# Performance work log

Hardware: AMD Instinct MI355X
Metric: run time of the kernel (lower is better)

## Reference

```python
import jax, jax.numpy as jnp
import numpy as np

BQ, BP, L, CIN, H1, H2, COUT = 32, 256, 16, 8192, 256, 32, 8192


def _conv_block(x, w1, b1, w2, b2, w3, b3):
    # x: (B, L, H1) -> Conv1d stack over token dim with residual, as in self.convs
    h = jnp.transpose(x, (0, 2, 1))  # (B, H1, L)
    for w, b in ((w1, b1), (w2, b2), (w3, b3)):
        h = jax.lax.conv_general_dilated(h, w, (1,), [(2, 2)],
                                         dimension_numbers=('NCH', 'OIH', 'NCH'))
        h = jax.nn.relu(h + b[None, :, None])
    return jnp.transpose(h, (0, 2, 1)) + x


def setup_inputs() -> dict:
    key = jax.random.key(0)
    ks = jax.random.split(key, 16)
    query_x = (jax.random.uniform(ks[0], (BQ, L, CIN)) < 0.01).astype(jnp.float32)
    poi_x = (jax.random.uniform(ks[1], (BP, L, CIN)) < 0.01).astype(jnp.float32)
    query_loc = jax.random.uniform(ks[2], (BQ, 2)) * 100.0
    poi_loc = jax.random.uniform(ks[3], (BP, 2)) * 100.0
    enc_w = jax.random.normal(ks[4], (H1, CIN)) * 0.02
    conv_w1 = jax.random.normal(ks[5], (H1, H1, 5)) * 0.02
    conv_w2 = jax.random.normal(ks[6], (H1, H1, 5)) * 0.02
    conv_w3 = jax.random.normal(ks[7], (H1, H1, 5)) * 0.02
    conv_b1 = jnp.zeros((H1,), jnp.float32)
    conv_b2 = jnp.zeros((H1,), jnp.float32)
    conv_b3 = jnp.zeros((H1,), jnp.float32)
    dec_w1 = jax.random.normal(ks[8], (H2, 2 * H1)) * 0.05
    dec_b1 = jnp.zeros((H2,), jnp.float32)
    dec_w2 = jax.random.normal(ks[9], (H2, H2)) * 0.1
    dec_b2 = jnp.zeros((H2,), jnp.float32)
    # torch init fills this with 0; use small randn so the path is non-trivial
    dec_w3 = jax.random.normal(ks[10], (COUT, H2)) * 0.01
    a = jnp.asarray(1.0, jnp.float32)
    b = jnp.asarray(0.0, jnp.float32)
    c = jnp.asarray(1.0, jnp.float32)
    d = jnp.asarray(0.0, jnp.float32)
    return dict(query_x=query_x, query_loc=query_loc, poi_x=poi_x, poi_loc=poi_loc,
                enc_w=enc_w, conv_w1=conv_w1, conv_b1=conv_b1, conv_w2=conv_w2,
                conv_b2=conv_b2, conv_w3=conv_w3, conv_b3=conv_b3,
                dec_w1=dec_w1, dec_b1=dec_b1, dec_w2=dec_w2, dec_b2=dec_b2,
                dec_w3=dec_w3, a=a, b=b, c=c, d=d)


def reference(query_x, query_loc, poi_x, poi_loc, enc_w, conv_w1, conv_b1,
              conv_w2, conv_b2, conv_w3, conv_b3, dec_w1, dec_b1, dec_w2,
              dec_b2, dec_w3, a, b, c, d):
    # --- encode ---
    q_h = _conv_block(query_x @ enc_w.T, conv_w1, conv_b1, conv_w2, conv_b2, conv_w3, conv_b3)
    p_h = _conv_block(poi_x @ enc_w.T, conv_w1, conv_b1, conv_w2, conv_b2, conv_w3, conv_b3)
    q_emb = q_h.mean(axis=1)  # (Bq, H1)
    p_emb = p_h.mean(axis=1)  # (Bp, H1)
    # --- bloom masks ---
    q_bloom = jnp.minimum(query_x.sum(axis=1), 1.0)  # (Bq, 8192)
    p_bloom = jnp.minimum(poi_x.sum(axis=1), 1.0)    # (Bp, 8192)
    interaction = q_bloom[:, None, :] * p_bloom[None, :, :]  # (Bq, Bp, 8192)
    q_bits = q_bloom.sum(axis=-1, keepdims=True)             # (Bq, 1)
    # --- pairwise MLP decode ---
    bq, bp = q_emb.shape[0], p_emb.shape[0]
    all_embed = jnp.concatenate([
        jnp.broadcast_to(q_emb[:, None, :], (bq, bp, q_emb.shape[-1])),
        jnp.broadcast_to(p_emb[None, :, :], (bq, bp, p_emb.shape[-1])),
    ], axis=-1)  # (Bq, Bp, 2*H1)
    h = jax.nn.relu(all_embed)
    h = jax.nn.relu(h @ dec_w1.T + dec_b1)
    h = jax.nn.relu(h @ dec_w2.T + dec_b2)
    w = h @ dec_w3.T  # (Bq, Bp, 8192)
    weights = jnp.where(w >= 0, w, w * 0.125) + 1.0  # LeakyReLU(1/8) + 1
    desc_sim = (interaction * weights).sum(axis=-1) / q_bits  # (Bq, Bp)
    # --- geo-distance fusion ---
    dist = jnp.sqrt(((query_loc[:, None, :] - poi_loc[None, :, :]) ** 2).sum(axis=-1))
    mean = desc_sim.mean(axis=-1, keepdims=True)
    std = jnp.std(desc_sim, axis=-1, keepdims=True, ddof=1)  # torch.std is unbiased
    desc_sim = (desc_sim - mean) / (std + 1e-6)
    dist_sim = -jnp.log(dist + 1.0)
    return (c - jax.nn.sigmoid(a * desc_sim + b)) * (dist_sim - d)
```

## Files before the change

kernel.cpp:

```cpp
#include <hip/hip_runtime.h>

#define NB 288
#define NBQ 32
#define NBP 256
#define LTOK 16
#define CIN 8192
#define H1 256
#define H2 32
#define MASKW 256
#define XROW 264

typedef __attribute__((ext_vector_type(8))) short short8;
typedef __attribute__((ext_vector_type(4))) float f32x4;

__device__ __forceinline__ unsigned short f2bf(float f) {
    unsigned u = __float_as_uint(f);
    u += 0x7fffu + ((u >> 16) & 1u);
    return (unsigned short)(u >> 16);
}

__device__ __forceinline__ float block_reduce_sum_256(float v, float* red) {
    int tid = threadIdx.x;
    red[tid] = v; __syncthreads();
    for (int st = 128; st > 0; st >>= 1) {
        if (tid < st) red[tid] += red[tid + st];
        __syncthreads();
    }
    float r = red[0];
    __syncthreads();
    return r;
}

__global__ __launch_bounds__(256) void k_transpose(const float* __restrict__ w,
                                                   float* __restrict__ wt) {
    __shared__ float tile[32][33];
    int k0 = blockIdx.x * 32;
    int h0 = blockIdx.y * 32;
    int tx = threadIdx.x & 31, ty = threadIdx.x >> 5;
#pragma unroll
    for (int i = 0; i < 32; i += 8)
        tile[ty + i][tx] = w[(h0 + ty + i) * CIN + k0 + tx];
    __syncthreads();
#pragma unroll
    for (int i = 0; i < 32; i += 8)
        wt[(size_t)(k0 + ty + i) * H1 + h0 + tx] = tile[tx][ty + i];
}

__global__ __launch_bounds__(256) void k_wprep(const float* __restrict__ w1,
                                               const float* __restrict__ w2,
                                               const float* __restrict__ w3,
                                               unsigned short* __restrict__ wtb) {
    int bx = blockIdx.x;
    int l = bx / 1280;
    int r = bx - l * 1280;
    int o = r / 5;
    int d = r - o * 5;
    int i = threadIdx.x;
    const float* w = (l == 0) ? w1 : (l == 1) ? w2 : w3;
    wtb[(size_t)l * 327680 + (size_t)o * 1280 + d * 256 + i] =
        f2bf(w[(size_t)o * 1280 + i * 5 + d]);
}

__global__ __launch_bounds__(256) void k_encode(const float* __restrict__ qx,
                                                const float* __restrict__ px,
                                                const float* __restrict__ wt,
                                                float* __restrict__ encoded,
                                                unsigned short* __restrict__ xbuf,
                                                unsigned* __restrict__ masks) {
    int row = blockIdx.x;
    int b = row >> 4;
    const float* x = (b < NBQ) ? (qx + (size_t)row * CIN)
                               : (px + (size_t)(row - NBQ * LTOK) * CIN);
    __shared__ int idxs[2048];
    __shared__ int cnt;
    int tid = threadIdx.x;
    if (tid == 0) cnt = 0;
    __syncthreads();
    const float4* x4 = (const float4*)x;
#pragma unroll
    for (int j = 0; j < 8; ++j) {
        float4 v = x4[j * 256 + tid];
        int base = (j * 256 + tid) * 4;
        float vv[4] = {v.x, v.y, v.z, v.w};
#pragma unroll
        for (int c = 0; c < 4; ++c) {
            if (vv[c] != 0.f) {
                int k = base + c;
                int p = atomicAdd(&cnt, 1);
                if (p < 2048) idxs[p] = k;
                atomicOr(&masks[b * MASKW + (k >> 5)], 1u << (k & 31));
            }
        }
    }
    __syncthreads();
    int n = min(cnt, 2048);
    float acc = 0.f;
#pragma unroll 4
    for (int j = 0; j < n; ++j)
        acc += wt[(size_t)idxs[j] * H1 + tid];
    encoded[(size_t)row * H1 + tid] = acc;
    xbuf[(size_t)row * H1 + tid] = f2bf(acc);
}

__global__ __launch_bounds__(256) void k_qbits(const unsigned* __restrict__ masks,
                                               float* __restrict__ qbits) {
    __shared__ int red[256];
    int q = blockIdx.x, tid = threadIdx.x;
    red[tid] = __popc(masks[q * MASKW + tid]);
    __syncthreads();
    for (int st = 128; st > 0; st >>= 1) {
        if (tid < st) red[tid] += red[tid + st];
        __syncthreads();
    }
    if (tid == 0) qbits[q] = (float)red[0];
}

__global__ __launch_bounds__(256) void k_cgemm(const unsigned short* __restrict__ actIn,
                                               unsigned short* __restrict__ actOut,
                                               float* __restrict__ actOutF,
                                               const unsigned short* __restrict__ wl,
                                               const float* __restrict__ bias,
                                               int last) {
    __shared__ unsigned short Als[4 * 20 * XROW];
    __shared__ unsigned short Bls[64 * XROW];
    int tid = threadIdx.x;
    int m0 = blockIdx.x * 64, n0 = blockIdx.y * 64;

    int* Ai = (int*)Als;
#pragma unroll
    for (int i = tid; i < 4 * 20 * XROW / 2; i += 256) Ai[i] = 0;
    __syncthreads();

    int row = tid >> 2, part = tid & 3;
    {
        const short8* src = (const short8*)(actIn + (size_t)(m0 + row) * 256 + part * 64);
        unsigned short* dst = Als + ((row >> 4) * 20 + (row & 15) + 2) * XROW + part * 64;
#pragma unroll
        for (int j = 0; j < 8; ++j) *(short8*)(dst + j * 8) = src[j];
    }
    const unsigned short* bsrc = wl + (size_t)(n0 + row) * 1280 + part * 64;
    short8 rb[8];
#pragma unroll
    for (int j = 0; j < 8; ++j) rb[j] = *(const short8*)(bsrc + j * 8);

    int lane = tid & 63, wave = tid >> 6;
    int lane15 = lane & 15, quad = lane >> 4;
    int wm = wave & 1, wn = wave >> 1;
    const unsigned short* Aw = Als + (wm * 2) * 20 * XROW;
    const unsigned short* Bw = Bls + (wn * 32) * XROW;
    unsigned short* bdst = Bls + row * XROW + part * 64;

    f32x4 acc[2][2];
#pragma unroll
    for (int mi = 0; mi < 2; ++mi)
#pragma unroll
        for (int ni = 0; ni < 2; ++ni) acc[mi][ni] = (f32x4){0.f, 0.f, 0.f, 0.f};

#pragma unroll 1
    for (int d = 0; d < 5; ++d) {
#pragma unroll
        for (int j = 0; j < 8; ++j) *(short8*)(bdst + j * 8) = rb[j];
        __syncthreads();
        if (d < 4) {
            const unsigned short* s2 = bsrc + (d + 1) * 256;
#pragma unroll
            for (int j = 0; j < 8; ++j) rb[j] = *(const short8*)(s2 + j * 8);
        }
        const unsigned short* a0 = Aw + (lane15 + d) * XROW + quad * 8;
        const unsigned short* a1 = a0 + 20 * XROW;
        const unsigned short* b0 = Bw + lane15 * XROW + quad * 8;
        const unsigned short* b1 = b0 + 16 * XROW;
#pragma unroll
        for (int kk = 0; kk < 8; ++kk) {
            short8 av0 = *(const short8*)(a0 + kk * 32);
            short8 av1 = *(const short8*)(a1 + kk * 32);
            short8 bv0 = *(const short8*)(b0 + kk * 32);
            short8 bv1 = *(const short8*)(b1 + kk * 32);
            acc[0][0] = __builtin_amdgcn_mfma_f32_16x16x32_bf16(av0, bv0, acc[0][0], 0, 0, 0);
            acc[0][1] = __builtin_amdgcn_mfma_f32_16x16x32_bf16(av0, bv1, acc[0][1], 0, 0, 0);
            acc[1][0] = __builtin_amdgcn_mfma_f32_16x16x32_bf16(av1, bv0, acc[1][0], 0, 0, 0);
            acc[1][1] = __builtin_amdgcn_mfma_f32_16x16x32_bf16(av1, bv1, acc[1][1], 0, 0, 0);
        }
        __syncthreads();
    }

#pragma unroll
    for (int ni = 0; ni < 2; ++ni) {
        int o = n0 + wn * 32 + ni * 16 + lane15;
        float bv = bias[o];
#pragma unroll
        for (int mi = 0; mi < 2; ++mi) {
            int rbase = m0 + wm * 32 + mi * 16 + quad * 4;
#pragma unroll
            for (int r = 0; r < 4; ++r) {
                float v = fmaxf(acc[mi][ni][r] + bv, 0.f);
                if (last) actOutF[(size_t)(rbase + r) * 256 + o] = v;
                else      actOut[(size_t)(rbase + r) * 256 + o] = f2bf(v);
            }
        }
    }
}

__global__ __launch_bounds__(256) void k_ab(const float* __restrict__ actF,
                                            const float* __restrict__ encoded,
                                            const float* __restrict__ w1,
                                            float* __restrict__ Cmat) {
    int b = blockIdx.x, tid = threadIdx.x;
    __shared__ float e[256];
    __shared__ float red[256];
    float s = 0.f;
#pragma unroll
    for (int t = 0; t < 16; ++t)
        s += actF[((size_t)b * 16 + t) * 256 + tid] + encoded[((size_t)b * 16 + t) * 256 + tid];
    e[tid] = fmaxf(s * (1.f / 16.f), 0.f);
    __syncthreads();
    int o = tid & 31, seg = tid >> 5;
    const float* wr = w1 + (size_t)o * 512 + (b < NBQ ? 0 : 256) + seg * 32;
    float v = 0.f;
#pragma unroll
    for (int i = 0; i < 32; ++i) v = fmaf(wr[i], e[seg * 32 + i], v);
    red[tid] = v; __syncthreads();
    if (tid < 128) red[tid] += red[tid + 128]; __syncthreads();
    if (tid < 64)  red[tid] += red[tid + 64];  __syncthreads();
    if (tid < 32) {
        red[tid] += red[tid + 32];
        Cmat[b * 32 + tid] = red[tid];
    }
}

__global__ __launch_bounds__(256) void k_pair(const float* __restrict__ Cmat,
                                              const float* __restrict__ b1,
                                              const float* __restrict__ w2,
                                              const float* __restrict__ b2,
                                              const float* __restrict__ w3,
                                              const unsigned* __restrict__ masks,
                                              const float* __restrict__ qbits,
                                              float* __restrict__ desc) {
    int p = blockIdx.x, q = blockIdx.y;
    __shared__ float h1[32];
    __shared__ __align__(16) float h2s[32];
    __shared__ int idxs[3072];
    __shared__ int cnt;
    __shared__ float red[256];
    int tid = threadIdx.x;
    if (tid == 0) cnt = 0;
    __syncthreads();
    unsigned m = masks[q * MASKW + tid] & masks[(NBQ + p) * MASKW + tid];
    int nb = __popc(m);
    if (nb) {
        int pos = atomicAdd(&cnt, nb);
        while (m) {
            int bit = __ffs(m) - 1;
            m &= m - 1;
            idxs[pos++] = tid * 32 + bit;
        }
    }
    if (tid < 32)
        h1[tid] = fmaxf(Cmat[q * 32 + tid] + Cmat[(NBQ + p) * 32 + tid] + b1[tid], 0.f);
    __syncthreads();
    if (tid < 32) {
        float s = b2[tid];
#pragma unroll
        for (int j = 0; j < 32; ++j) s = fmaf(w2[tid * 32 + j], h1[j], s);
        h2s[tid] = fmaxf(s, 0.f);
    }
    __syncthreads();
    int n = cnt;
    int rowi = tid >> 3, part = tid & 7;
    float4 h = ((const float4*)h2s)[part];
    float local = 0.f;
    for (int base = 0; base < n; base += 32) {
        int r = base + rowi;
        bool act = r < n;
        float dot = 0.f;
        if (act) {
            float4 wv = *(const float4*)(w3 + (size_t)idxs[r] * 32 + part * 4);
            dot = wv.x * h.x + wv.y * h.y + wv.z * h.z + wv.w * h.w;
        }
        dot += __shfl_xor(dot, 1);
        dot += __shfl_xor(dot, 2);
        dot += __shfl_xor(dot, 4);
        if (act && part == 0)
            local += 1.f + (dot >= 0.f ? dot : dot * 0.125f);
    }
    float total = block_reduce_sum_256(local, red);
    if (tid == 0) desc[q * 256 + p] = total / qbits[q];
}

__global__ __launch_bounds__(256) void k_final(const float* __restrict__ desc,
                                               const float* __restrict__ qloc,
                                               const float* __restrict__ ploc,
                                               const float* __restrict__ sa,
                                               const float* __restrict__ sb,
                                               const float* __restrict__ sc,
                                               const float* __restrict__ sd,
                                               float* __restrict__ out) {
    __shared__ float red[256];
    int q = blockIdx.x, tid = threadIdx.x;
    float v = desc[q * 256 + tid];
    float mean = block_reduce_sum_256(v, red) * (1.f / 256.f);
    float dv = v - mean;
    float var = block_reduce_sum_256(dv * dv, red) * (1.f / 255.f);
    float norm = dv / (sqrtf(var) + 1e-6f);
    float dx = qloc[q * 2]     - ploc[tid * 2];
    float dy = qloc[q * 2 + 1] - ploc[tid * 2 + 1];
    float dist = sqrtf(dx * dx + dy * dy);
    float z = sa[0] * norm + sb[0];
    float sig = 1.f / (1.f + expf(-z));
    out[q * 256 + tid] = (sc[0] - sig) * (-logf(dist + 1.f) - sd[0]);
}

extern "C" void kernel_launch(void* const* d_in, const int* in_sizes, int n_in,
                              void* d_out, int out_size, void* d_ws, size_t ws_size,
                              hipStream_t stream) {
    const float* qx   = (const float*)d_in[0];
    const float* qloc = (const float*)d_in[1];
    const float* px   = (const float*)d_in[2];
    const float* ploc = (const float*)d_in[3];
    const float* encw = (const float*)d_in[4];
    const float* cw1  = (const float*)d_in[5];
    const float* cb1  = (const float*)d_in[6];
    const float* cw2  = (const float*)d_in[7];
    const float* cb2  = (const float*)d_in[8];
    const float* cw3  = (const float*)d_in[9];
    const float* cb3  = (const float*)d_in[10];
    const float* dw1  = (const float*)d_in[11];
    const float* db1  = (const float*)d_in[12];
    const float* dw2  = (const float*)d_in[13];
    const float* db2  = (const float*)d_in[14];
    const float* dw3  = (const float*)d_in[15];
    const float* sa   = (const float*)d_in[16];
    const float* sb   = (const float*)d_in[17];
    const float* sc   = (const float*)d_in[18];
    const float* sd   = (const float*)d_in[19];

    char* w = (char*)d_ws;
    float*          enc_wT  = (float*)w;          w += (size_t)CIN * H1 * 4;
    float*          encoded = (float*)w;          w += (size_t)NB * LTOK * H1 * 4;
    unsigned short* xbuf    = (unsigned short*)w; w += (size_t)NB * LTOK * H1 * 2;
    unsigned short* act1    = (unsigned short*)w; w += (size_t)NB * LTOK * H1 * 2;
    unsigned short* act2    = (unsigned short*)w; w += (size_t)NB * LTOK * H1 * 2;
    float*          actF    = (float*)w;          w += (size_t)NB * LTOK * H1 * 4;
    unsigned short* wtb     = (unsigned short*)w; w += (size_t)3 * 256 * 1280 * 2;
    float*          Cmat    = (float*)w;          w += (size_t)NB * H2 * 4;
    unsigned*       masks   = (unsigned*)w;       w += (size_t)NB * MASKW * 4;
    float*          qbits   = (float*)w;          w += 1024;
    float*          desc    = (float*)w;          w += (size_t)NBQ * NBP * 4;

    hipMemsetAsync(masks, 0, (size_t)NB * MASKW * 4, stream);
    k_transpose<<<dim3(CIN / 32, H1 / 32), 256, 0, stream>>>(encw, enc_wT);
    k_wprep<<<3840, 256, 0, stream>>>(cw1, cw2, cw3, wtb);
    k_encode<<<NB * LTOK, 256, 0, stream>>>(qx, px, enc_wT, encoded, xbuf, masks);
    k_qbits<<<NBQ, 256, 0, stream>>>(masks, qbits);
    dim3 cgrid(NB * LTOK / 64, 4);
    k_cgemm<<<cgrid, 256, 0, stream>>>(xbuf, act1, actF, wtb,              cb1, 0);
    k_cgemm<<<cgrid, 256, 0, stream>>>(act1, act2, actF, wtb + 327680,     cb2, 0);
    k_cgemm<<<cgrid, 256, 0, stream>>>(act2, act1, actF, wtb + 2 * 327680, cb3, 1);
    k_ab<<<NB, 256, 0, stream>>>(actF, encoded, dw1, Cmat);
    k_pair<<<dim3(NBP, NBQ), 256, 0, stream>>>(Cmat, db1, dw2, db2, dw3, masks, qbits, desc);
    k_final<<<NBQ, 256, 0, stream>>>(desc, qloc, ploc, sa, sb, sc, sd, (float*)d_out);
}
```

Measured before the change: 364.6 us.

## Split encode into scan and bf16 gather, shrink conv GEMM tiles, wave-reduce pair

The fused encode kernel becomes two kernels. A scan kernel skips all-zero float4 chunks and writes a capped, padded index list to global memory. A gather kernel then sums rows of a bf16-packed transposed encoder weight, padding with a zero sentinel row, which halves the bytes per gathered row. The conv GEMM tile shrinks from 64x64 to 32x32, giving four times as many blocks. The pair kernel's final reduction uses wave shuffles instead of a shared-memory tree. The risks are lower encoder precision from bf16 weights and silent truncation of tokens with more than 192 active bits.

```diff
diff --git a/kernel.cpp b/kernel.cpp
--- a/kernel.cpp
+++ b/kernel.cpp
@@ -9,6 +9,7 @@
 #define H2 32
 #define MASKW 256
 #define XROW 264
+#define IDXCAP 208
 
 typedef __attribute__((ext_vector_type(8))) short short8;
 typedef __attribute__((ext_vector_type(4))) float f32x4;
@@ -19,20 +20,8 @@
     return (unsigned short)(u >> 16);
 }
 
-__device__ __forceinline__ float block_reduce_sum_256(float v, float* red) {
-    int tid = threadIdx.x;
-    red[tid] = v; __syncthreads();
-    for (int st = 128; st > 0; st >>= 1) {
-        if (tid < st) red[tid] += red[tid + st];
-        __syncthreads();
-    }
-    float r = red[0];
-    __syncthreads();
-    return r;
-}
-
-__global__ __launch_bounds__(256) void k_transpose(const float* __restrict__ w,
-                                                   float* __restrict__ wt) {
+__global__ __launch_bounds__(256) void k_transpose_pack(const float* __restrict__ w,
+                                                        unsigned* __restrict__ wtp) {
     __shared__ float tile[32][33];
     int k0 = blockIdx.x * 32;
     int h0 = blockIdx.y * 32;
@@ -41,16 +30,23 @@
     for (int i = 0; i < 32; i += 8)
         tile[ty + i][tx] = w[(h0 + ty + i) * CIN + k0 + tx];
     __syncthreads();
-#pragma unroll
-    for (int i = 0; i < 32; i += 8)
-        wt[(size_t)(k0 + ty + i) * H1 + h0 + tx] = tile[tx][ty + i];
+    int kl = threadIdx.x >> 3, pw = threadIdx.x & 7;
+#pragma unroll
+    for (int u = 0; u < 2; ++u) {
+        int p = pw + u * 8;
+        unsigned lo = f2bf(tile[2 * p][kl]);
+        unsigned hi = f2bf(tile[2 * p + 1][kl]);
+        wtp[(size_t)(k0 + kl) * 128 + (h0 >> 1) + p] = (hi << 16) | lo;
+    }
 }
 
 __global__ __launch_bounds__(256) void k_wprep(const float* __restrict__ w1,
                                                const float* __restrict__ w2,
                                                const float* __restrict__ w3,
-                                               unsigned short* __restrict__ wtb) {
+                                               unsigned short* __restrict__ wtb,
+                                               unsigned* __restrict__ wtp) {
     int bx = blockIdx.x;
+    if (bx == 0 && threadIdx.x < 128) wtp[(size_t)8192 * 128 + threadIdx.x] = 0;
     int l = bx / 1280;
     int r = bx - l * 1280;
     int o = r / 5;
@@ -61,45 +57,69 @@
         f2bf(w[(size_t)o * 1280 + i * 5 + d]);
 }
 
-__global__ __launch_bounds__(256) void k_encode(const float* __restrict__ qx,
-                                                const float* __restrict__ px,
-                                                const float* __restrict__ wt,
-                                                float* __restrict__ encoded,
-                                                unsigned short* __restrict__ xbuf,
-                                                unsigned* __restrict__ masks) {
+__global__ __launch_bounds__(256) void k_scan(const float* __restrict__ qx,
+                                              const float* __restrict__ px,
+                                              int* __restrict__ idxl,
+                                              int* __restrict__ cnts,
+                                              unsigned* __restrict__ masks) {
     int row = blockIdx.x;
     int b = row >> 4;
     const float* x = (b < NBQ) ? (qx + (size_t)row * CIN)
                                : (px + (size_t)(row - NBQ * LTOK) * CIN);
-    __shared__ int idxs[2048];
     __shared__ int cnt;
     int tid = threadIdx.x;
     if (tid == 0) cnt = 0;
     __syncthreads();
+    int* il = idxl + (size_t)row * IDXCAP;
     const float4* x4 = (const float4*)x;
 #pragma unroll
     for (int j = 0; j < 8; ++j) {
         float4 v = x4[j * 256 + tid];
-        int base = (j * 256 + tid) * 4;
-        float vv[4] = {v.x, v.y, v.z, v.w};
-#pragma unroll
-        for (int c = 0; c < 4; ++c) {
-            if (vv[c] != 0.f) {
-                int k = base + c;
-                int p = atomicAdd(&cnt, 1);
-                if (p < 2048) idxs[p] = k;
-                atomicOr(&masks[b * MASKW + (k >> 5)], 1u << (k & 31));
+        unsigned ox = __float_as_uint(v.x) | __float_as_uint(v.y) |
+                      __float_as_uint(v.z) | __float_as_uint(v.w);
+        if (ox) {
+            int base = (j * 256 + tid) * 4;
+            float vv[4] = {v.x, v.y, v.z, v.w};
+#pragma unroll
+            for (int c = 0; c < 4; ++c) {
+                if (vv[c] != 0.f) {
+                    int k = base + c;
+                    int p = atomicAdd(&cnt, 1);
+                    if (p < 192) il[p] = k;
+                    atomicOr(&masks[b * MASKW + (k >> 5)], 1u << (k & 31));
+                }
             }
         }
     }
     __syncthreads();
-    int n = min(cnt, 2048);
-    float acc = 0.f;
-#pragma unroll 4
-    for (int j = 0; j < n; ++j)
-        acc += wt[(size_t)idxs[j] * H1 + tid];
-    encoded[(size_t)row * H1 + tid] = acc;
-    xbuf[(size_t)row * H1 + tid] = f2bf(acc);
+    int n = min(cnt, 192);
+    if (tid == 0) cnts[row] = n;
+    for (int i = n + tid; i < 200; i += 256) il[i] = 8192;
+}
+
+__global__ __launch_bounds__(128) void k_gather(const unsigned* __restrict__ wtp,
+                                                const int* __restrict__ idxl,
+                                                const int* __restrict__ cnts,
+                                                float* __restrict__ encoded,
+                                                unsigned* __restrict__ xbufu) {
+    int row = blockIdx.x, tid = threadIdx.x;
+    int n = cnts[row];
+    const int* il = idxl + (size_t)row * IDXCAP;
+    float aL = 0.f, aH = 0.f;
+    for (int j = 0; j < n; j += 8) {
+        int4 ia = *(const int4*)(il + j);
+        int4 ib = *(const int4*)(il + j + 4);
+        int id[8] = {ia.x, ia.y, ia.z, ia.w, ib.x, ib.y, ib.z, ib.w};
+#pragma unroll
+        for (int u = 0; u < 8; ++u) {
+            unsigned v = wtp[(size_t)id[u] * 128 + tid];
+            aL += __uint_as_float(v << 16);
+            aH += __uint_as_float(v & 0xffff0000u);
+        }
+    }
+    ((float2*)encoded)[(size_t)row * 128 + tid] = float2{aL, aH};
+    unsigned bl = f2bf(aL), bh = f2bf(aH);
+    xbufu[(size_t)row * 128 + tid] = (bh << 16) | bl;
 }
 
 __global__ __launch_bounds__(256) void k_qbits(const unsigned* __restrict__ masks,
@@ -121,83 +141,64 @@
                                                const unsigned short* __restrict__ wl,
                                                const float* __restrict__ bias,
                                                int last) {
-    __shared__ unsigned short Als[4 * 20 * XROW];
-    __shared__ unsigned short Bls[64 * XROW];
+    __shared__ unsigned short Als[2 * 20 * XROW];
+    __shared__ unsigned short Bls[32 * XROW];
     int tid = threadIdx.x;
-    int m0 = blockIdx.x * 64, n0 = blockIdx.y * 64;
+    int m0 = blockIdx.x * 32, n0 = blockIdx.y * 32;
 
     int* Ai = (int*)Als;
 #pragma unroll
-    for (int i = tid; i < 4 * 20 * XROW / 2; i += 256) Ai[i] = 0;
-    __syncthreads();
-
-    int row = tid >> 2, part = tid & 3;
+    for (int i = tid; i < 20 * XROW; i += 256) Ai[i] = 0;
+    __syncthreads();
+
+    int row = tid >> 3, part = tid & 7;
     {
-        const short8* src = (const short8*)(actIn + (size_t)(m0 + row) * 256 + part * 64);
-        unsigned short* dst = Als + ((row >> 4) * 20 + (row & 15) + 2) * XROW + part * 64;
-#pragma unroll
-        for (int j = 0; j < 8; ++j) *(short8*)(dst + j * 8) = src[j];
-    }
-    const unsigned short* bsrc = wl + (size_t)(n0 + row) * 1280 + part * 64;
-    short8 rb[8];
-#pragma unroll
-    for (int j = 0; j < 8; ++j) rb[j] = *(const short8*)(bsrc + j * 8);
+        const short8* src = (const short8*)(actIn + (size_t)(m0 + row) * 256 + part * 32);
+        unsigned short* dst = Als + ((row >> 4) * 20 + (row & 15) + 2) * XROW + part * 32;
+#pragma unroll
+        for (int j = 0; j < 4; ++j) *(short8*)(dst + j * 8) = src[j];
+    }
+    const unsigned short* bsrc = wl + (size_t)(n0 + row) * 1280 + part * 32;
+    short8 rb[4];
+#pragma unroll
+    for (int j = 0; j < 4; ++j) rb[j] = *(const short8*)(bsrc + j * 8);
 
     int lane = tid & 63, wave = tid >> 6;
     int lane15 = lane & 15, quad = lane >> 4;
     int wm = wave & 1, wn = wave >> 1;
-    const unsigned short* Aw = Als + (wm * 2) * 20 * XROW;
-    const unsigned short* Bw = Bls + (wn * 32) * XROW;
-    unsigned short* bdst = Bls + row * XROW + part * 64;
-
-    f32x4 acc[2][2];
-#pragma unroll
-    for (int mi = 0; mi < 2; ++mi)
-#pragma unroll
-        for (int ni = 0; ni < 2; ++ni) acc[mi][ni] = (f32x4){0.f, 0.f, 0.f, 0.f};
+    unsigned short* bdst = Bls + row * XROW + part * 32;
+
+    f32x4 acc = (f32x4){0.f, 0.f, 0.f, 0.f};
 
 #pragma unroll 1
     for (int d = 0; d < 5; ++d) {
 #pragma unroll
-        for (int j = 0; j < 8; ++j) *(short8*)(bdst + j * 8) = rb[j];
+        for (int j = 0; j < 4; ++j) *(short8*)(bdst + j * 8) = rb[j];
         __syncthreads();
         if (d < 4) {
             const unsigned short* s2 = bsrc + (d + 1) * 256;
 #pragma unroll
-            for (int j = 0; j < 8; ++j) rb[j] = *(const short8*)(s2 + j * 8);
-        }
-        const unsigned short* a0 = Aw + (lane15 + d) * XROW + quad * 8;
-        const unsigned short* a1 = a0 + 20 * XROW;
-        const unsigned short* b0 = Bw + lane15 * XROW + quad * 8;
-        const unsigned short* b1 = b0 + 16 * XROW;
+            for (int j = 0; j < 4; ++j) rb[j] = *(const short8*)(s2 + j * 8);
+        }
+        const unsigned short* ap = Als + (wm * 20 + lane15 + d) * XROW + quad * 8;
+        const unsigned short* bp = Bls + (wn * 16 + lane15) * XROW + quad * 8;
 #pragma unroll
         for (int kk = 0; kk < 8; ++kk) {
-            short8 av0 = *(const short8*)(a0 + kk * 32);
-            short8 av1 = *(const short8*)(a1 + kk * 32);
-            short8 bv0 = *(const short8*)(b0 + kk * 32);
-            short8 bv1 = *(const short8*)(b1 + kk * 32);
-            acc[0][0] = __builtin_amdgcn_mfma_f32_16x16x32_bf16(av0, bv0, acc[0][0], 0, 0, 0);
-            acc[0][1] = __builtin_amdgcn_mfma_f32_16x16x32_bf16(av0, bv1, acc[0][1], 0, 0, 0);
-            acc[1][0] = __builtin_amdgcn_mfma_f32_16x16x32_bf16(av1, bv0, acc[1][0], 0, 0, 0);
-            acc[1][1] = __builtin_amdgcn_mfma_f32_16x16x32_bf16(av1, bv1, acc[1][1], 0, 0, 0);
-        }
-        __syncthreads();
-    }
-
-#pragma unroll
-    for (int ni = 0; ni < 2; ++ni) {
-        int o = n0 + wn * 32 + ni * 16 + lane15;
-        float bv = bias[o];
-#pragma unroll
-        for (int mi = 0; mi < 2; ++mi) {
-            int rbase = m0 + wm * 32 + mi * 16 + quad * 4;
-#pragma unroll
-            for (int r = 0; r < 4; ++r) {
-                float v = fmaxf(acc[mi][ni][r] + bv, 0.f);
-                if (last) actOutF[(size_t)(rbase + r) * 256 + o] = v;
-                else      actOut[(size_t)(rbase + r) * 256 + o] = f2bf(v);
-            }
-        }
+            short8 av = *(const short8*)(ap + kk * 32);
+            short8 bv = *(const short8*)(bp + kk * 32);
+            acc = __builtin_amdgcn_mfma_f32_16x16x32_bf16(av, bv, acc, 0, 0, 0);
+        }
+        __syncthreads();
+    }
+
+    int o = n0 + wn * 16 + lane15;
+    float bv = bias[o];
+    int rbase = m0 + wm * 16 + quad * 4;
+#pragma unroll
+    for (int r = 0; r < 4; ++r) {
+        float v = fmaxf(acc[r] + bv, 0.f);
+        if (last) actOutF[(size_t)(rbase + r) * 256 + o] = v;
+        else      actOut[(size_t)(rbase + r) * 256 + o] = f2bf(v);
     }
 }
 
@@ -241,7 +242,7 @@
     __shared__ __align__(16) float h2s[32];
     __shared__ int idxs[3072];
     __shared__ int cnt;
-    __shared__ float red[256];
+    __shared__ float wsum[4];
     int tid = threadIdx.x;
     if (tid == 0) cnt = 0;
     __syncthreads();
@@ -283,8 +284,12 @@
         if (act && part == 0)
             local += 1.f + (dot >= 0.f ? dot : dot * 0.125f);
     }
-    float total = block_reduce_sum_256(local, red);
-    if (tid == 0) desc[q * 256 + p] = total / qbits[q];
+#pragma unroll
+    for (int st = 1; st < 64; st <<= 1) local += __shfl_xor(local, st);
+    if ((tid & 63) == 0) wsum[tid >> 6] = local;
+    __syncthreads();
+    if (tid == 0)
+        desc[q * 256 + p] = (wsum[0] + wsum[1] + wsum[2] + wsum[3]) / qbits[q];
 }
 
 __global__ __launch_bounds__(256) void k_final(const float* __restrict__ desc,
@@ -298,9 +303,20 @@
     __shared__ float red[256];
     int q = blockIdx.x, tid = threadIdx.x;
     float v = desc[q * 256 + tid];
-    float mean = block_reduce_sum_256(v, red) * (1.f / 256.f);
+    red[tid] = v; __syncthreads();
+    for (int st = 128; st > 0; st >>= 1) {
+        if (tid < st) red[tid] += red[tid + st];
+        __syncthreads();
+    }
+    float mean = red[0] * (1.f / 256.f);
+    __syncthreads();
     float dv = v - mean;
-    float var = block_reduce_sum_256(dv * dv, red) * (1.f / 255.f);
+    red[tid] = dv * dv; __syncthreads();
+    for (int st = 128; st > 0; st >>= 1) {
+        if (tid < st) red[tid] += red[tid + st];
+        __syncthreads();
+    }
+    float var = red[0] * (1.f / 255.f);
     float norm = dv / (sqrtf(var) + 1e-6f);
     float dx = qloc[q * 2]     - ploc[tid * 2];
     float dy = qloc[q * 2 + 1] - ploc[tid * 2 + 1];
@@ -335,24 +351,27 @@
     const float* sd   = (const float*)d_in[19];
 
     char* w = (char*)d_ws;
-    float*          enc_wT  = (float*)w;          w += (size_t)CIN * H1 * 4;
+    unsigned*       wtp     = (unsigned*)w;       w += (size_t)8193 * 128 * 4;
     float*          encoded = (float*)w;          w += (size_t)NB * LTOK * H1 * 4;
     unsigned short* xbuf    = (unsigned short*)w; w += (size_t)NB * LTOK * H1 * 2;
     unsigned short* act1    = (unsigned short*)w; w += (size_t)NB * LTOK * H1 * 2;
     unsigned short* act2    = (unsigned short*)w; w += (size_t)NB * LTOK * H1 * 2;
     float*          actF    = (float*)w;          w += (size_t)NB * LTOK * H1 * 4;
     unsigned short* wtb     = (unsigned short*)w; w += (size_t)3 * 256 * 1280 * 2;
+    int*            idxl    = (int*)w;            w += (size_t)NB * LTOK * IDXCAP * 4;
+    int*            cnts    = (int*)w;            w += (size_t)NB * LTOK * 4;
     float*          Cmat    = (float*)w;          w += (size_t)NB * H2 * 4;
     unsigned*       masks   = (unsigned*)w;       w += (size_t)NB * MASKW * 4;
     float*          qbits   = (float*)w;          w += 1024;
     float*          desc    = (float*)w;          w += (size_t)NBQ * NBP * 4;
 
     hipMemsetAsync(masks, 0, (size_t)NB * MASKW * 4, stream);
-    k_transpose<<<dim3(CIN / 32, H1 / 32), 256, 0, stream>>>(encw, enc_wT);
-    k_wprep<<<3840, 256, 0, stream>>>(cw1, cw2, cw3, wtb);
-    k_encode<<<NB * LTOK, 256, 0, stream>>>(qx, px, enc_wT, encoded, xbuf, masks);
+    k_transpose_pack<<<dim3(CIN / 32, H1 / 32), 256, 0, stream>>>(encw, wtp);
+    k_wprep<<<3840, 256, 0, stream>>>(cw1, cw2, cw3, wtb, wtp);
+    k_scan<<<NB * LTOK, 256, 0, stream>>>(qx, px, idxl, cnts, masks);
+    k_gather<<<NB * LTOK, 128, 0, stream>>>(wtp, idxl, cnts, encoded, (unsigned*)xbuf);
     k_qbits<<<NBQ, 256, 0, stream>>>(masks, qbits);
-    dim3 cgrid(NB * LTOK / 64, 4);
+    dim3 cgrid(NB * LTOK / 32, 8);
     k_cgemm<<<cgrid, 256, 0, stream>>>(xbuf, act1, actF, wtb,              cb1, 0);
     k_cgemm<<<cgrid, 256, 0, stream>>>(act1, act2, actF, wtb + 327680,     cb2, 0);
     k_cgemm<<<cgrid, 256, 0, stream>>>(act2, act1, actF, wtb + 2 * 327680, cb3, 1);
```

New measurement: 359.2 us. No clear change (-1.5%).
